# Kernel optimization log

Hardware: AMD Instinct MI355X
Metric: run time of the kernel (lower is better)

Reference implementation:

```python
import jax, jax.numpy as jnp
import numpy as np

H = 64

def _gru(x, Wih, Whh, bih, bhh):
    # x: [NB, L, D]; torch GRU gate order: r, z, n
    h0 = jnp.zeros((x.shape[0], Whh.shape[1]), x.dtype)
    def step(h, xt):
        gi = xt @ Wih.T + bih
        gh = h @ Whh.T + bhh
        ir, iz, inn = jnp.split(gi, 3, axis=-1)
        hr, hz, hn = jnp.split(gh, 3, axis=-1)
        r = jax.nn.sigmoid(ir + hr)
        z = jax.nn.sigmoid(iz + hz)
        n = jnp.tanh(inn + r * hn)
        h_new = (1.0 - z) * n + z * h
        return h_new, h_new
    hT, ys = jax.lax.scan(step, h0, jnp.swapaxes(x, 0, 1))
    return jnp.swapaxes(ys, 0, 1), hT  # outputs [NB,L,H], last hidden [NB,H]


def setup_inputs() -> dict:
    key = jax.random.key(0)
    ks = jax.random.split(key, 20)
    N, B, L, D = 2000, 8, 12, 2
    E = 16000
    s = 0.1
    return {
        "data": jax.random.normal(ks[0], (N, B, L, D), jnp.float32),
        "features": jax.random.normal(ks[1], (N, H), jnp.float32),
        "edge_index": jax.random.randint(ks[2], (2, E), 0, N, jnp.int64 if jax.config.jax_enable_x64 else jnp.int32),
        "Wih1": jax.random.normal(ks[3], (3 * H, D), jnp.float32) * s,
        "Whh1": jax.random.normal(ks[4], (3 * H, H), jnp.float32) * s,
        "bih1": jax.random.normal(ks[5], (3 * H,), jnp.float32) * s,
        "bhh1": jax.random.normal(ks[6], (3 * H,), jnp.float32) * s,
        "W1": jax.random.normal(ks[7], (16, 2 * H), jnp.float32) * s,
        "b1": jax.random.normal(ks[8], (16,), jnp.float32) * s,
        "W2": jax.random.normal(ks[9], (2, 16), jnp.float32) * s,
        "b2": jax.random.normal(ks[10], (2,), jnp.float32) * s,
        "W3": jax.random.normal(ks[11], (2 * H * H, 2), jnp.float32) * s,
        "b3": jax.random.normal(ks[12], (2 * H * H,), jnp.float32) * s,
        "Wih2": jax.random.normal(ks[13], (3 * H, H), jnp.float32) * s,
        "Whh2": jax.random.normal(ks[14], (3 * H, H), jnp.float32) * s,
        "bih2": jax.random.normal(ks[15], (3 * H,), jnp.float32) * s,
        "bhh2": jax.random.normal(ks[16], (3 * H,), jnp.float32) * s,
    }


def reference(data, features, edge_index, Wih1, Whh1, bih1, bhh1,
              W1, b1, W2, b2, W3, b3, Wih2, Whh2, bih2, bhh2):
    N, B, L, D = data.shape
    # --- first GRU over [N*B, L, D] ---
    out1, h1 = _gru(data.reshape(N * B, L, D), Wih1, Whh1, bih1, bhh1)
    out1 = out1.reshape(N, B, L, H)
    h1 = h1.reshape(N, B, H)
    # --- MetaGAT with self loops ---
    loops = jnp.arange(N, dtype=edge_index.dtype)
    src = jnp.concatenate([edge_index[0], loops])  # j (source)
    dst = jnp.concatenate([edge_index[1], loops])  # i (target)
    states_j = out1[src]                 # [E', B, L, H]
    states_i = out1[dst]
    feats = jnp.concatenate([features[dst], features[src]], axis=-1)  # [E', 2H]
    # per-edge MLP generating weights
    hdn = jax.nn.sigmoid(feats @ W1.T + b1)
    hdn = jax.nn.sigmoid(hdn @ W2.T + b2)
    w = (hdn @ W3.T + b3).reshape(-1, 2 * H, H)  # [E', 2H, H]
    states = jnp.concatenate([states_i, states_j], axis=-1)  # [E', B, L, 2H]
    alpha = jax.nn.leaky_relu(jnp.einsum('eblk,ekh->eblh', states, w))
    alpha = jax.nn.softmax(alpha, axis=1)  # softmax over batch dim, as in source
    msg = alpha * states_j                 # [E', B, L, H]
    agg = jax.ops.segment_sum(msg, dst, num_segments=N)
    out2 = jax.nn.relu(agg)                # [N, B, L, H]
    # --- second GRU ---
    _, h2 = _gru(out2.reshape(N * B, L, H), Wih2, Whh2, bih2, bhh2)
    h2 = h2.reshape(N, B, H)
    return h1, h2
```

## Files before the change

### kernel.cpp

```cpp
#include <hip/hip_runtime.h>
#include <hip/hip_bf16.h>

typedef unsigned short ushort_t;
typedef unsigned int uint_t;
typedef __attribute__((ext_vector_type(8))) short bf16x8;
typedef __attribute__((ext_vector_type(4))) float f32x4;

#define NNODE 2000
#define NB 8
#define LSEQ 12
#define HDIM 64
#define NEDGE 16000
#define NSEQ (NNODE * NB)
#define OUT1_ELEMS (NNODE * NB * LSEQ * HDIM)
#define OUT1_BYTES (OUT1_ELEMS * 2)
#define AGG_BYTES  (OUT1_ELEMS * 2)
#define SST 72
#define LOG2E 1.4426950408889634f

#define WFRAG_ELEMS (6 * 2 * 256 * 8)
#define G2FRAG_ELEMS (3 * 2 * 2 * 256 * 8)

__device__ __forceinline__ float bf1(ushort_t u) { return __uint_as_float(((uint_t)u) << 16); }
__device__ __forceinline__ ushort_t fbf(float f) {
    uint_t x = __float_as_uint(f);
    uint_t r = x + 0x7fffu + ((x >> 16) & 1u);
    return (ushort_t)(r >> 16);
}
__device__ __forceinline__ float sigm(float x) {
    return __builtin_amdgcn_rcpf(1.f + __expf(-x));
}
__device__ __forceinline__ float sigm2(float x) {
    return __builtin_amdgcn_rcpf(1.f + __builtin_amdgcn_exp2f(-x));
}
__device__ __forceinline__ float tanh2(float x) {
    return 2.f * __builtin_amdgcn_rcpf(1.f + __builtin_amdgcn_exp2f(-x)) - 1.f;
}


__global__ __launch_bounds__(256) void mega_kernel(
    const float* __restrict__ data, const float* __restrict__ Wih,
    const float* __restrict__ Whh, const float* __restrict__ bih,
    const float* __restrict__ bhh, ushort_t* __restrict__ out1,
    float* __restrict__ h1out,
    const int* __restrict__ edges, int* __restrict__ degree,
    int* __restrict__ rowstart, int* __restrict__ srcids,
    int* __restrict__ eids, int* __restrict__ order,
    const float* __restrict__ features,
    const float* __restrict__ W1, const float* __restrict__ b1,
    const float* __restrict__ W2, const float* __restrict__ b2,
    float* __restrict__ alphas,
    const float* __restrict__ W3, const float* __restrict__ b3,
    const float* __restrict__ Wih2, const float* __restrict__ Whh2,
    ushort_t* __restrict__ wfrag, ushort_t* __restrict__ g2frag)
{
    __shared__ ushort_t H[2][16][SST] __attribute__((aligned(16)));
    __shared__ float XD[16][26];
    __shared__ int hist[NNODE];
    __shared__ int wsum[4];
    __shared__ float m1[4][16];
    __shared__ int dh[64];

    const int bx = blockIdx.x;
    const int tid = threadIdx.x;

    if (bx == 5501) {
        {
            const int wv = tid >> 6, r = tid & 15, quad = (tid >> 4) & 3;
            const int n = wv * 16 + r;
#pragma unroll
            for (int ks = 0; ks < 2; ++ks) {
                ushort_t ta[8], tb[8], tc[8], ba[8], bb[8], bc[8];
#pragma unroll
                for (int jj = 0; jj < 8; ++jj) {
                    const int mt_ = (ks * 32 + quad * 8 + jj) * 64 + n;
                    float2 w2 = ((const float2*)W3)[mt_];
                    ta[jj] = fbf(w2.x * LOG2E); tb[jj] = fbf(w2.y * LOG2E);
                    tc[jj] = fbf(b3[mt_] * LOG2E);
                    const int mb_ = (64 + ks * 32 + quad * 8 + jj) * 64 + n;
                    float2 w2b = ((const float2*)W3)[mb_];
                    ba[jj] = fbf(w2b.x * LOG2E); bb[jj] = fbf(w2b.y * LOG2E);
                    bc[jj] = fbf(b3[mb_] * LOG2E);
                }
                *(uint4*)(wfrag + ((0 * 2 + ks) * 256 + tid) * 8) = *(uint4*)ta;
                *(uint4*)(wfrag + ((1 * 2 + ks) * 256 + tid) * 8) = *(uint4*)tb;
                *(uint4*)(wfrag + ((2 * 2 + ks) * 256 + tid) * 8) = *(uint4*)tc;
                *(uint4*)(wfrag + ((3 * 2 + ks) * 256 + tid) * 8) = *(uint4*)ba;
                *(uint4*)(wfrag + ((4 * 2 + ks) * 256 + tid) * 8) = *(uint4*)bb;
                *(uint4*)(wfrag + ((5 * 2 + ks) * 256 + tid) * 8) = *(uint4*)bc;
            }
        }
        {
            const int nw = tid >> 6, c = tid & 15, quad = (tid >> 4) & 3;
            const int j = nw * 16 + c;
#pragma unroll
            for (int g = 0; g < 3; ++g) {
                const float sc = (g == 2) ? 2.f * LOG2E : LOG2E;
                const int row = g * 64 + j;
#pragma unroll
                for (int ks = 0; ks < 2; ++ks) {
                    const float* wp = Whh2 + (row << 6) + ks * 32 + quad * 8;
                    float4 wa = *(const float4*)wp;
                    float4 wb = *(const float4*)(wp + 4);
                    ushort_t tmp[8];
                    tmp[0] = fbf(wa.x * sc); tmp[1] = fbf(wa.y * sc);
                    tmp[2] = fbf(wa.z * sc); tmp[3] = fbf(wa.w * sc);
                    tmp[4] = fbf(wb.x * sc); tmp[5] = fbf(wb.y * sc);
                    tmp[6] = fbf(wb.z * sc); tmp[7] = fbf(wb.w * sc);
                    *(uint4*)(g2frag + (((g * 2 + ks) * 2 + 0) * 256 + tid) * 8) = *(uint4*)tmp;
                    const float* wp2 = Wih2 + (row << 6) + ks * 32 + quad * 8;
                    float4 va = *(const float4*)wp2;
                    float4 vb = *(const float4*)(wp2 + 4);
                    tmp[0] = fbf(va.x * sc); tmp[1] = fbf(va.y * sc);
                    tmp[2] = fbf(va.z * sc); tmp[3] = fbf(va.w * sc);
                    tmp[4] = fbf(vb.x * sc); tmp[5] = fbf(vb.y * sc);
                    tmp[6] = fbf(vb.z * sc); tmp[7] = fbf(vb.w * sc);
                    *(uint4*)(g2frag + (((g * 2 + ks) * 2 + 1) * 256 + tid) * 8) = *(uint4*)tmp;
                }
            }
        }
        return;
    }

    if (bx == 1000) {
        for (int k = tid; k < NNODE; k += 256) hist[k] = 0;
        if (tid < 64) dh[tid] = 0;
        __syncthreads();
        for (int it = 0; it < 16; ++it) {
            const int e0 = it * 1024 + tid * 4;
            if (e0 + 3 < NEDGE) {
                int4 v4 = *(const int4*)(edges + NEDGE + e0);
                atomicAdd(&hist[v4.x], 1);
                atomicAdd(&hist[v4.y], 1);
                atomicAdd(&hist[v4.z], 1);
                atomicAdd(&hist[v4.w], 1);
            } else {
#pragma unroll
                for (int k = 0; k < 4; ++k) {
                    const int e = e0 + k;
                    if (e < NEDGE) atomicAdd(&hist[edges[NEDGE + e]], 1);
                }
            }
        }
        __syncthreads();
        const int lane = tid & 63, w = tid >> 6;
        int d[8];
        int s = 0;
#pragma unroll
        for (int q = 0; q < 8; ++q) {
            const int idx = tid * 8 + q;
            d[q] = (idx < NNODE) ? hist[idx] : 0;
            s += d[q];
        }
        int v = s;
#pragma unroll
        for (int off = 1; off < 64; off <<= 1) {
            int u = __shfl_up(v, off);
            if (lane >= off) v += u;
        }
        if (lane == 63) wsum[w] = v;
        __syncthreads();
        int base = 0;
        for (int k = 0; k < 4; ++k) if (k < w) base += wsum[k];
        int run = base + v - s;
        int rs8[8];
#pragma unroll
        for (int q = 0; q < 8; ++q) {
            const int idx = tid * 8 + q;
            if (idx < NNODE) {
                rs8[q] = run;
                rowstart[idx] = run;
                degree[idx] = d[q];
                run += d[q];
                atomicAdd(&dh[63 - min(d[q], 63)], 1);
            }
        }
        __syncthreads();
        if (tid == 0) {
            int acc = 0;
            for (int k = 0; k < 64; ++k) { const int c = dh[k]; dh[k] = acc; acc += c; }
        }
        __syncthreads();
#pragma unroll
        for (int q = 0; q < 8; ++q) {
            const int idx = tid * 8 + q;
            if (idx < NNODE) {
                const int pos = atomicAdd(&dh[63 - min(d[q], 63)], 1);
                order[pos] = idx;
            }
        }
        __syncthreads();
#pragma unroll
        for (int q = 0; q < 8; ++q) {
            const int idx = tid * 8 + q;
            if (idx < NNODE) hist[idx] = rs8[q];
        }
        __syncthreads();
        for (int it = 0; it < 16; ++it) {
            const int e0 = it * 1024 + tid * 4;
            if (e0 + 3 < NEDGE) {
                int4 dv4 = *(const int4*)(edges + NEDGE + e0);
                int4 sv4 = *(const int4*)(edges + e0);
                int pos;
                pos = atomicAdd(&hist[dv4.x], 1); srcids[pos] = sv4.x; eids[pos] = e0;
                pos = atomicAdd(&hist[dv4.y], 1); srcids[pos] = sv4.y; eids[pos] = e0 + 1;
                pos = atomicAdd(&hist[dv4.z], 1); srcids[pos] = sv4.z; eids[pos] = e0 + 2;
                pos = atomicAdd(&hist[dv4.w], 1); srcids[pos] = sv4.w; eids[pos] = e0 + 3;
            } else {
#pragma unroll
                for (int k = 0; k < 4; ++k) {
                    const int e = e0 + k;
                    if (e < NEDGE) {
                        const int pos = atomicAdd(&hist[edges[NEDGE + e]], 1);
                        srcids[pos] = edges[e];
                        eids[pos] = e;
                    }
                }
            }
        }
        return;
    }

    if (bx > 1000) {
        const int w = tid >> 6, lane = tid & 63;
        const int e = (bx - 1001) * 4 + w;
        int i, j;
        if (e < NEDGE) { j = edges[e]; i = edges[NEDGE + e]; }
        else { i = j = e - NEDGE; }
        const int o = lane >> 2, q = lane & 3;
        const float* fsrc = (q < 2) ? (features + i * 64 + q * 32)
                                    : (features + j * 64 + (q - 2) * 32);
        const float* wsrc = W1 + o * 128 + q * 32;
        const float4* f4 = (const float4*)fsrc;
        const float4* w4 = (const float4*)wsrc;
        float acc = 0.f;
#pragma unroll
        for (int k = 0; k < 8; ++k) {
            float4 a = f4[k], b = w4[k];
            acc = fmaf(a.x, b.x, acc);
            acc = fmaf(a.y, b.y, acc);
            acc = fmaf(a.z, b.z, acc);
            acc = fmaf(a.w, b.w, acc);
        }
        acc += __shfl_xor(acc, 1);
        acc += __shfl_xor(acc, 2);
        if (q == 0) m1[w][o] = sigm(acc + b1[o]);
        __syncthreads();
        if (lane < 32 && e < NEDGE + NNODE) {
            const int o2 = lane >> 4, k = lane & 15;
            float p = m1[w][k] * W2[o2 * 16 + k];
            p += __shfl_xor(p, 1);
            p += __shfl_xor(p, 2);
            p += __shfl_xor(p, 4);
            p += __shfl_xor(p, 8);
            if (k == 0) alphas[e * 2 + o2] = sigm(p + b2[o2]);
        }
        return;
    }

    const int nw = tid >> 6;
    const int c = tid & 15;
    const int quad = (tid >> 4) & 3;
    const int j = nw * 16 + c;
    const int s0 = bx * 16;
    const int crow = tid >> 4, ccol = (tid & 15) * 4;

    if (tid < 128) *(uint4*)&H[0][tid >> 3][(tid & 7) * 8] = uint4{0, 0, 0, 0};
#pragma unroll
    for (int p = 0; p < 2; ++p) {
        const int flat = p * 256 + tid;
        if (flat < 384) {
            const int sl = flat / 24, q = flat - sl * 24;
            XD[sl][q] = data[(s0 + sl) * 24 + q];
        }
    }

    bf16x8 Bh[3][2];
    float wi0[3], wi1[3], bi[3], bh[3];
#pragma unroll
    for (int g = 0; g < 3; ++g) {
        const float sc = (g == 2) ? 2.f * LOG2E : LOG2E;
        const int row = g * 64 + j;
        float2 wi = *(const float2*)(Wih + row * 2);
        wi0[g] = wi.x * sc; wi1[g] = wi.y * sc;
        bi[g] = bih[row] * sc; bh[g] = bhh[row] * sc;
#pragma unroll
        for (int ks = 0; ks < 2; ++ks) {
            const float* wp = Whh + (row << 6) + ks * 32 + quad * 8;
            float4 wa = *(const float4*)wp;
            float4 wb = *(const float4*)(wp + 4);
            ushort_t tmp[8];
            tmp[0] = fbf(wa.x * sc); tmp[1] = fbf(wa.y * sc);
            tmp[2] = fbf(wa.z * sc); tmp[3] = fbf(wa.w * sc);
            tmp[4] = fbf(wb.x * sc); tmp[5] = fbf(wb.y * sc);
            tmp[6] = fbf(wb.z * sc); tmp[7] = fbf(wb.w * sc);
            Bh[g][ks] = *(bf16x8*)tmp;
        }
    }

    float hold[4];
#pragma unroll
    for (int rg = 0; rg < 4; ++rg) hold[rg] = 0.f;

    for (int t = 0; t < LSEQ; ++t) {
        __syncthreads();
        const ushort_t (*Hr)[SST] = H[t & 1];
        ushort_t (*Hw)[SST] = H[1 - (t & 1)];
        bf16x8 a0 = *(const bf16x8*)&Hr[c][quad * 8];
        bf16x8 a1 = *(const bf16x8*)&Hr[c][32 + quad * 8];
        if (t > 0)
            *(uint2*)(out1 + (s0 + crow) * (LSEQ * HDIM) + (t - 1) * HDIM + ccol) =
                *(const uint2*)&Hr[crow][ccol];
        f32x4 gh[3];
#pragma unroll
        for (int g = 0; g < 3; ++g) {
            f32x4 acc = {0.f, 0.f, 0.f, 0.f};
            acc = __builtin_amdgcn_mfma_f32_16x16x32_bf16(a0, Bh[g][0], acc, 0, 0, 0);
            acc = __builtin_amdgcn_mfma_f32_16x16x32_bf16(a1, Bh[g][1], acc, 0, 0, 0);
            gh[g] = acc;
        }
#pragma unroll
        for (int rg = 0; rg < 4; ++rg) {
            const int sloc = quad * 4 + rg;
            float2 xp = *(const float2*)&XD[sloc][2 * t];
            float gr = bh[0] + gh[0][rg];
            float gz = bh[1] + gh[1][rg];
            float gn = bh[2] + gh[2][rg];
            float ir = bi[0] + wi0[0] * xp.x + wi1[0] * xp.y;
            float iz = bi[1] + wi0[1] * xp.x + wi1[1] * xp.y;
            float in = bi[2] + wi0[2] * xp.x + wi1[2] * xp.y;
            float r = sigm2(ir + gr);
            float z = sigm2(iz + gz);
            float n = tanh2(in + r * gn);
            float hv = (1.f - z) * n + z * hold[rg];
            hold[rg] = hv;
            Hw[sloc][j] = fbf(hv);
        }
    }
    __syncthreads();
    *(uint2*)(out1 + (s0 + crow) * (LSEQ * HDIM) + (LSEQ - 1) * HDIM + ccol) =
        *(const uint2*)&H[LSEQ & 1][crow][ccol];
#pragma unroll
    for (int rg = 0; rg < 4; ++rg) {
        const int sloc = quad * 4 + rg;
        h1out[(s0 + sloc) * HDIM + j] = hold[rg];
    }
}

__global__ __launch_bounds__(256) void gat_csr_kernel(
    const ushort_t* __restrict__ out1,
    const int* __restrict__ degree, const int* __restrict__ rowstart,
    const int* __restrict__ srcids, const int* __restrict__ eids,
    const int* __restrict__ order,
    const float* __restrict__ alphas,
    const ushort_t* __restrict__ wfrag,
    ushort_t* __restrict__ agg)
{
    __shared__ ushort_t POOL[4][32][SST] __attribute__((aligned(16)));

    const int tid = threadIdx.x;
    const int i = order[blockIdx.x];
    const int mh = blockIdx.y;
    const int deg = degree[i];
    const int rs = rowstart[i];

    const int wv = tid >> 6;
    const int r = tid & 15;
    const int quad = (tid >> 4) & 3;
    const int n = wv * 16 + r;

    const float2 aSelf = *(const float2*)(alphas + (NEDGE + i) * 2);

    int glo[2], lso[2];
#pragma unroll
    for (int p = 0; p < 2; ++p) {
        const int u = p * 256 + tid;
        const int rr = u >> 4, c4 = u & 15;
        const int b = rr & 7, l = (rr >> 3) + 4 * mh;
        glo[p] = (b * 12 + l) * 64 + c4 * 4;
        lso[p] = rr * SST + c4 * 4;
    }
    int afo[2][2];
#pragma unroll
    for (int mt = 0; mt < 2; ++mt) {
        afo[mt][0] = (mt * 16 + r) * SST + quad * 8;
        afo[mt][1] = afo[mt][0] + 32;
    }
    int cbo[2];
#pragma unroll
    for (int mt = 0; mt < 2; ++mt)
        cbo[mt] = (mt * 16 + quad * 4) * SST + (n & ~1);
    const uint_t shamt = (n & 1) ? 0u : 16u;

    const ushort_t* pi = out1 + i * (NB * LSEQ * HDIM);
    ushort_t* const sbase = &POOL[0][0][0];
    ushort_t* const Si = sbase;

#pragma unroll
    for (int p = 0; p < 2; ++p)
        *(uint2*)(Si + lso[p]) = *(const uint2*)(pi + glo[p]);

    bf16x8 WtA[2], WtB[2], WtC[2], WbA[2], WbB[2], WbC[2];
#pragma unroll
    for (int ks = 0; ks < 2; ++ks) {
        WtA[ks] = *(const bf16x8*)(wfrag + ((0 * 2 + ks) * 256 + tid) * 8);
        WtB[ks] = *(const bf16x8*)(wfrag + ((1 * 2 + ks) * 256 + tid) * 8);
        WtC[ks] = *(const bf16x8*)(wfrag + ((2 * 2 + ks) * 256 + tid) * 8);
        WbA[ks] = *(const bf16x8*)(wfrag + ((3 * 2 + ks) * 256 + tid) * 8);
        WbB[ks] = *(const bf16x8*)(wfrag + ((4 * 2 + ks) * 256 + tid) * 8);
        WbC[ks] = *(const bf16x8*)(wfrag + ((5 * 2 + ks) * 256 + tid) * 8);
    }

    __syncthreads();

    f32x4 PA[2], PB[2], PC[2];
#pragma unroll
    for (int mt = 0; mt < 2; ++mt) {
        bf16x8 af0 = *(const bf16x8*)(Si + afo[mt][0]);
        bf16x8 af1 = *(const bf16x8*)(Si + afo[mt][1]);
        f32x4 pa = {0.f, 0.f, 0.f, 0.f};
        f32x4 pb = {0.f, 0.f, 0.f, 0.f};
        f32x4 pc = {0.f, 0.f, 0.f, 0.f};
        pa = __builtin_amdgcn_mfma_f32_16x16x32_bf16(af0, WtA[0], pa, 0, 0, 0);
        pa = __builtin_amdgcn_mfma_f32_16x16x32_bf16(af1, WtA[1], pa, 0, 0, 0);
        pb = __builtin_amdgcn_mfma_f32_16x16x32_bf16(af0, WtB[0], pb, 0, 0, 0);
        pb = __builtin_amdgcn_mfma_f32_16x16x32_bf16(af1, WtB[1], pb, 0, 0, 0);
        pc = __builtin_amdgcn_mfma_f32_16x16x32_bf16(af0, WtC[0], pc, 0, 0, 0);
        pc = __builtin_amdgcn_mfma_f32_16x16x32_bf16(af1, WtC[1], pc, 0, 0, 0);
        PA[mt] = pa; PB[mt] = pb; PC[mt] = pc;
    }

    float accN[2][4];
#pragma unroll
    for (int mt = 0; mt < 2; ++mt)
#pragma unroll
        for (int g2 = 0; g2 < 4; ++g2) accN[mt][g2] = 0.f;

    auto process = [&](const ushort_t* SB, float2 a01) {
#pragma unroll
        for (int mt = 0; mt < 2; ++mt) {
            bf16x8 aj0 = *(const bf16x8*)(SB + afo[mt][0]);
            bf16x8 aj1 = *(const bf16x8*)(SB + afo[mt][1]);
            const uint_t* dp = (const uint_t*)(SB + cbo[mt]);
            uint_t d0 = dp[0], d1 = dp[36], d2 = dp[72], d3 = dp[108];
            f32x4 aA = PA[mt], aB = PB[mt], aC = PC[mt];
            aA = __builtin_amdgcn_mfma_f32_16x16x32_bf16(aj0, WbA[0], aA, 0, 0, 0);
            aA = __builtin_amdgcn_mfma_f32_16x16x32_bf16(aj1, WbA[1], aA, 0, 0, 0);
            aB = __builtin_amdgcn_mfma_f32_16x16x32_bf16(aj0, WbB[0], aB, 0, 0, 0);
            aB = __builtin_amdgcn_mfma_f32_16x16x32_bf16(aj1, WbB[1], aB, 0, 0, 0);
            aC = __builtin_amdgcn_mfma_f32_16x16x32_bf16(aj0, WbC[0], aC, 0, 0, 0);
            aC = __builtin_amdgcn_mfma_f32_16x16x32_bf16(aj1, WbC[1], aC, 0, 0, 0);
            float v[4];
            float s = 0.f;
#pragma unroll
            for (int g2 = 0; g2 < 4; ++g2) {
                float x = fmaf(a01.x, aA[g2], fmaf(a01.y, aB[g2], aC[g2]));
                x = fmaxf(x, 0.01f * x);
                v[g2] = __builtin_amdgcn_exp2f(x);
                s += v[g2];
            }
            s += __shfl_xor(s, 16);
            const float inv = __builtin_amdgcn_rcpf(s);
            uint_t dd[4] = {d0, d1, d2, d3};
#pragma unroll
            for (int g2 = 0; g2 < 4; ++g2) {
                const float sj = __uint_as_float((dd[g2] << shamt) & 0xFFFF0000u);
                accN[mt][g2] += v[g2] * inv * sj;
            }
        }
    };

    int eA1 = 0, eB1 = 0, eA2 = 0, eB2 = 0, sa2 = 0, sb2 = 0;
    float2 aA_cur = float2{0.f, 0.f}, aB_cur = float2{0.f, 0.f};
    if (deg >= 1) aA_cur = *(const float2*)(alphas + eids[rs] * 2);
    if (deg >= 2) aB_cur = *(const float2*)(alphas + eids[rs + 1] * 2);
    if (deg >= 3) eA1 = eids[rs + 2];
    if (deg >= 4) eB1 = eids[rs + 3];
    if (deg >= 5) { eA2 = eids[rs + 4]; sa2 = srcids[rs + 4]; }
    if (deg >= 6) { eB2 = eids[rs + 5]; sb2 = srcids[rs + 5]; }

    uint2 pfEA[2], pfEB[2], pfOA[2], pfOB[2];
    {
        const ushort_t* pA = out1 + ((deg >= 1) ? srcids[rs]     : 0) * (NB * LSEQ * HDIM);
        const ushort_t* pB = out1 + ((deg >= 2) ? srcids[rs + 1] : 0) * (NB * LSEQ * HDIM);
        const ushort_t* pC = out1 + ((deg >= 3) ? srcids[rs + 2] : 0) * (NB * LSEQ * HDIM);
        const ushort_t* pD = out1 + ((deg >= 4) ? srcids[rs + 3] : 0) * (NB * LSEQ * HDIM);
#pragma unroll
        for (int p = 0; p < 2; ++p) {
            pfEA[p] = *(const uint2*)(pA + glo[p]);
            pfEB[p] = *(const uint2*)(pB + glo[p]);
            pfOA[p] = *(const uint2*)(pC + glo[p]);
            pfOB[p] = *(const uint2*)(pD + glo[p]);
        }
    }

    process(Si, aSelf);
    __syncthreads();

    const int npairs = (deg + 1) >> 1;
    for (int pk = 0; pk < npairs; ++pk) {
        const int base = pk * 2;
        ushort_t* SA = sbase + (2 * (pk & 1)) * (32 * SST);
        ushort_t* SB = SA + 32 * SST;

        if ((pk & 1) == 0) {
#pragma unroll
            for (int p = 0; p < 2; ++p) {
                *(uint2*)(SA + lso[p]) = pfEA[p];
                *(uint2*)(SB + lso[p]) = pfEB[p];
            }
            if (base + 4 < deg) {
                const ushort_t* pA = out1 + sa2 * (NB * LSEQ * HDIM);
#pragma unroll
                for (int p = 0; p < 2; ++p) pfEA[p] = *(const uint2*)(pA + glo[p]);
            }
            if (base + 5 < deg) {
                const ushort_t* pB = out1 + sb2 * (NB * LSEQ * HDIM);
#pragma unroll
                for (int p = 0; p < 2; ++p) pfEB[p] = *(const uint2*)(pB + glo[p]);
            }
        } else {
#pragma unroll
            for (int p = 0; p < 2; ++p) {
                *(uint2*)(SA + lso[p]) = pfOA[p];
                *(uint2*)(SB + lso[p]) = pfOB[p];
            }
            if (base + 4 < deg) {
                const ushort_t* pA = out1 + sa2 * (NB * LSEQ * HDIM);
#pragma unroll
                for (int p = 0; p < 2; ++p) pfOA[p] = *(const uint2*)(pA + glo[p]);
            }
            if (base + 5 < deg) {
                const ushort_t* pB = out1 + sb2 * (NB * LSEQ * HDIM);
#pragma unroll
                for (int p = 0; p < 2; ++p) pfOB[p] = *(const uint2*)(pB + glo[p]);
            }
        }

        int sa_nw = 0, sb_nw = 0, e3A = 0, e3B = 0;
        if (base + 6 < deg) { sa_nw = srcids[rs + base + 6]; e3A = eids[rs + base + 6]; }
        if (base + 7 < deg) { sb_nw = srcids[rs + base + 7]; e3B = eids[rs + base + 7]; }
        float2 aA_n = float2{0.f, 0.f}, aB_n = float2{0.f, 0.f};
        if (base + 2 < deg) aA_n = *(const float2*)(alphas + eA1 * 2);
        if (base + 3 < deg) aB_n = *(const float2*)(alphas + eB1 * 2);

        __syncthreads();

        process(SA, aA_cur);
        if (base + 1 < deg) process(SB, aB_cur);

        aA_cur = aA_n; aB_cur = aB_n;
        eA1 = eA2; eB1 = eB2; eA2 = e3A; eB2 = e3B;
        sa2 = sa_nw; sb2 = sb_nw;
    }

#pragma unroll
    for (int mt = 0; mt < 2; ++mt)
#pragma unroll
        for (int g2 = 0; g2 < 4; ++g2) {
            const int gr = mh * 32 + mt * 16 + quad * 4 + g2;
            const int b = gr & 7, l = gr >> 3;
            agg[(i * 96 + b * 12 + l) * 64 + n] = fbf(accN[mt][g2]);
        }
}

__global__ __launch_bounds__(256) void gru2_kernel(
    const ushort_t* __restrict__ agg, const ushort_t* __restrict__ g2frag,
    const float* __restrict__ bih, const float* __restrict__ bhh,
    float* __restrict__ h2out)
{
    __shared__ ushort_t H[2][16][SST] __attribute__((aligned(16)));
    __shared__ ushort_t X[2][16][SST] __attribute__((aligned(16)));

    const int tid = threadIdx.x;
    const int nw = tid >> 6;
    const int c = tid & 15;
    const int quad = (tid >> 4) & 3;
    const int j = nw * 16 + c;
    const int s0 = blockIdx.x * 16;
    const int sl = tid >> 3, k0 = (tid & 7) * 8;

    if (tid < 128) *(uint4*)&H[0][tid >> 3][(tid & 7) * 8] = uint4{0, 0, 0, 0};

    bf16x8 Bh[3][2], Bi[3][2];
    float bi[3], bh[3];
#pragma unroll
    for (int g = 0; g < 3; ++g) {
        const float sc = (g == 2) ? 2.f * LOG2E : LOG2E;
        const int row = g * 64 + j;
        bi[g] = bih[row] * sc; bh[g] = bhh[row] * sc;
#pragma unroll
        for (int ks = 0; ks < 2; ++ks) {
            Bh[g][ks] = *(const bf16x8*)(g2frag + (((g * 2 + ks) * 2 + 0) * 256 + tid) * 8);
            Bi[g][ks] = *(const bf16x8*)(g2frag + (((g * 2 + ks) * 2 + 1) * 256 + tid) * 8);
        }
    }

    float hold[4];
#pragma unroll
    for (int rg = 0; rg < 4; ++rg) hold[rg] = 0.f;

    if (tid < 128) {
        ushort_t xr[8];
        *(uint4*)xr = *(const uint4*)(agg + (s0 + sl) * (LSEQ * HDIM) + k0);
        ushort_t xs[8];
#pragma unroll
        for (int q = 0; q < 8; ++q) xs[q] = (xr[q] & 0x8000u) ? (ushort_t)0 : xr[q];
        *(uint4*)&X[0][sl][k0] = *(uint4*)xs;
    }

    for (int t = 0; t < LSEQ; ++t) {
        __syncthreads();
        const int rb = t & 1, wb = 1 - rb;
        bf16x8 ah0 = *(const bf16x8*)&H[rb][c][quad * 8];
        bf16x8 ah1 = *(const bf16x8*)&H[rb][c][32 + quad * 8];
        bf16x8 ax0 = *(const bf16x8*)&X[rb][c][quad * 8];
        bf16x8 ax1 = *(const bf16x8*)&X[rb][c][32 + quad * 8];

        ushort_t xr[8];
        if (t < LSEQ - 1 && tid < 128)
            *(uint4*)xr = *(const uint4*)(agg + (s0 + sl) * (LSEQ * HDIM) +
                                          (t + 1) * HDIM + k0);

        f32x4 gh[3], gi[3];
#pragma unroll
        for (int g = 0; g < 3; ++g) {
            f32x4 acc = {0.f, 0.f, 0.f, 0.f};
            acc = __builtin_amdgcn_mfma_f32_16x16x32_bf16(ah0, Bh[g][0], acc, 0, 0, 0);
            acc = __builtin_amdgcn_mfma_f32_16x16x32_bf16(ah1, Bh[g][1], acc, 0, 0, 0);
            gh[g] = acc;
            f32x4 acc2 = {0.f, 0.f, 0.f, 0.f};
            acc2 = __builtin_amdgcn_mfma_f32_16x16x32_bf16(ax0, Bi[g][0], acc2, 0, 0, 0);
            acc2 = __builtin_amdgcn_mfma_f32_16x16x32_bf16(ax1, Bi[g][1], acc2, 0, 0, 0);
            gi[g] = acc2;
        }
#pragma unroll
        for (int rg = 0; rg < 4; ++rg) {
            const int sloc = quad * 4 + rg;
            float r = sigm2(bi[0] + gi[0][rg] + bh[0] + gh[0][rg]);
            float z = sigm2(bi[1] + gi[1][rg] + bh[1] + gh[1][rg]);
            float n = tanh2(bi[2] + gi[2][rg] + r * (bh[2] + gh[2][rg]));
            float hv = (1.f - z) * n + z * hold[rg];
            hold[rg] = hv;
            H[wb][sloc][j] = fbf(hv);
        }
        if (t < LSEQ - 1 && tid < 128) {
            ushort_t xs[8];
#pragma unroll
            for (int q = 0; q < 8; ++q) xs[q] = (xr[q] & 0x8000u) ? (ushort_t)0 : xr[q];
            *(uint4*)&X[wb][sl][k0] = *(uint4*)xs;
        }
    }
#pragma unroll
    for (int rg = 0; rg < 4; ++rg) {
        const int sloc = quad * 4 + rg;
        h2out[(s0 + sloc) * HDIM + j] = hold[rg];
    }
}

extern "C" void kernel_launch(void* const* d_in, const int* in_sizes, int n_in,
                              void* d_out, int out_size, void* d_ws, size_t ws_size,
                              hipStream_t stream)
{
    const float* data     = (const float*)d_in[0];
    const float* features = (const float*)d_in[1];
    const int*   edges    = (const int*)d_in[2];
    const float* Wih1     = (const float*)d_in[3];
    const float* Whh1     = (const float*)d_in[4];
    const float* bih1     = (const float*)d_in[5];
    const float* bhh1     = (const float*)d_in[6];
    const float* W1       = (const float*)d_in[7];
    const float* b1       = (const float*)d_in[8];
    const float* W2       = (const float*)d_in[9];
    const float* b2       = (const float*)d_in[10];
    const float* W3       = (const float*)d_in[11];
    const float* b3       = (const float*)d_in[12];
    const float* Wih2     = (const float*)d_in[13];
    const float* Whh2     = (const float*)d_in[14];
    const float* bih2     = (const float*)d_in[15];
    const float* bhh2     = (const float*)d_in[16];

    float*    out  = (float*)d_out;
    char*     ws   = (char*)d_ws;
    ushort_t* out1 = (ushort_t*)ws;
    ushort_t* agg  = (ushort_t*)(ws + OUT1_BYTES);
    int*      meta = (int*)(ws + OUT1_BYTES + AGG_BYTES);
    int*   degree   = meta;
    int*   rowstart = meta + NNODE;
    int*   srcids   = meta + 2 * NNODE;
    int*   eids     = meta + 2 * NNODE + NEDGE;
    int*   order    = meta + 2 * NNODE + 2 * NEDGE;
    float* alphas   = (float*)(meta + 3 * NNODE + 2 * NEDGE);
    ushort_t* wfrag  = (ushort_t*)((char*)alphas + 36000 * 4);
    ushort_t* g2frag = wfrag + WFRAG_ELEMS;

    mega_kernel<<<1001 + 4500 + 1, 256, 0, stream>>>(
        data, Wih1, Whh1, bih1, bhh1, out1, out,
        edges, degree, rowstart, srcids, eids, order,
        features, W1, b1, W2, b2, alphas,
        W3, b3, Wih2, Whh2, wfrag, g2frag);
    gat_csr_kernel<<<dim3(NNODE, 3), 256, 0, stream>>>(out1, degree, rowstart, srcids,
                                                       eids, order, alphas, wfrag, agg);
    gru2_kernel<<<NSEQ / 16, 256, 0, stream>>>(agg, g2frag, bih2, bhh2,
                                               out + NNODE * NB * HDIM);
}
```

Measured before the change: 230.7 us.

## Process GAT neighbor edges in groups of four with double-buffered LDS

Restructures the per-node GAT edge loop to stage four neighbor tiles per iteration instead of two. LDS is doubled to 8 buffers and prefetches of the next four source tiles are issued after the barrier. This halves the number of __syncthreads per node and exposes more memory-level parallelism for the gathers. The cost is more registers for the prefetched tiles, more LDS per block (lower occupancy), and some wasted work on low-degree nodes.

```diff
diff --git a/kernel.cpp b/kernel.cpp
--- a/kernel.cpp
+++ b/kernel.cpp
@@ -356,7 +356,7 @@
     const ushort_t* __restrict__ wfrag,
     ushort_t* __restrict__ agg)
 {
-    __shared__ ushort_t POOL[4][32][SST] __attribute__((aligned(16)));
+    __shared__ ushort_t POOL[8][32][SST] __attribute__((aligned(16)));
 
     const int tid = threadIdx.x;
     const int i = order[blockIdx.x];
@@ -409,6 +409,25 @@
         WbA[ks] = *(const bf16x8*)(wfrag + ((3 * 2 + ks) * 256 + tid) * 8);
         WbB[ks] = *(const bf16x8*)(wfrag + ((4 * 2 + ks) * 256 + tid) * 8);
         WbC[ks] = *(const bf16x8*)(wfrag + ((5 * 2 + ks) * 256 + tid) * 8);
+    }
+
+    float2 aC[4];
+    int e1[4], s1[4];
+#pragma unroll
+    for (int k = 0; k < 4; ++k) {
+        aC[k] = float2{0.f, 0.f};
+        if (k < deg) aC[k] = *(const float2*)(alphas + eids[rs + k] * 2);
+        const int idx = 4 + k;
+        e1[k] = 0; s1[k] = 0;
+        if (idx < deg) { e1[k] = eids[rs + idx]; s1[k] = srcids[rs + idx]; }
+    }
+
+    uint2 pf[4][2];
+#pragma unroll
+    for (int k = 0; k < 4; ++k) {
+        const ushort_t* pA = out1 + ((k < deg) ? srcids[rs + k] : 0) * (NB * LSEQ * HDIM);
+#pragma unroll
+        for (int p = 0; p < 2; ++p) pf[k][p] = *(const uint2*)(pA + glo[p]);
     }
 
     __syncthreads();
@@ -443,18 +462,18 @@
             bf16x8 aj1 = *(const bf16x8*)(SB + afo[mt][1]);
             const uint_t* dp = (const uint_t*)(SB + cbo[mt]);
             uint_t d0 = dp[0], d1 = dp[36], d2 = dp[72], d3 = dp[108];
-            f32x4 aA = PA[mt], aB = PB[mt], aC = PC[mt];
+            f32x4 aA = PA[mt], aB = PB[mt], aC_ = PC[mt];
             aA = __builtin_amdgcn_mfma_f32_16x16x32_bf16(aj0, WbA[0], aA, 0, 0, 0);
             aA = __builtin_amdgcn_mfma_f32_16x16x32_bf16(aj1, WbA[1], aA, 0, 0, 0);
             aB = __builtin_amdgcn_mfma_f32_16x16x32_bf16(aj0, WbB[0], aB, 0, 0, 0);
             aB = __builtin_amdgcn_mfma_f32_16x16x32_bf16(aj1, WbB[1], aB, 0, 0, 0);
-            aC = __builtin_amdgcn_mfma_f32_16x16x32_bf16(aj0, WbC[0], aC, 0, 0, 0);
-            aC = __builtin_amdgcn_mfma_f32_16x16x32_bf16(aj1, WbC[1], aC, 0, 0, 0);
+            aC_ = __builtin_amdgcn_mfma_f32_16x16x32_bf16(aj0, WbC[0], aC_, 0, 0, 0);
+            aC_ = __builtin_amdgcn_mfma_f32_16x16x32_bf16(aj1, WbC[1], aC_, 0, 0, 0);
             float v[4];
             float s = 0.f;
 #pragma unroll
             for (int g2 = 0; g2 < 4; ++g2) {
-                float x = fmaf(a01.x, aA[g2], fmaf(a01.y, aB[g2], aC[g2]));
+                float x = fmaf(a01.x, aA[g2], fmaf(a01.y, aB[g2], aC_[g2]));
                 x = fmaxf(x, 0.01f * x);
                 v[g2] = __builtin_amdgcn_exp2f(x);
                 s += v[g2];
@@ -470,88 +489,52 @@
         }
     };
 
-    int eA1 = 0, eB1 = 0, eA2 = 0, eB2 = 0, sa2 = 0, sb2 = 0;
-    float2 aA_cur = float2{0.f, 0.f}, aB_cur = float2{0.f, 0.f};
-    if (deg >= 1) aA_cur = *(const float2*)(alphas + eids[rs] * 2);
-    if (deg >= 2) aB_cur = *(const float2*)(alphas + eids[rs + 1] * 2);
-    if (deg >= 3) eA1 = eids[rs + 2];
-    if (deg >= 4) eB1 = eids[rs + 3];
-    if (deg >= 5) { eA2 = eids[rs + 4]; sa2 = srcids[rs + 4]; }
-    if (deg >= 6) { eB2 = eids[rs + 5]; sb2 = srcids[rs + 5]; }
-
-    uint2 pfEA[2], pfEB[2], pfOA[2], pfOB[2];
-    {
-        const ushort_t* pA = out1 + ((deg >= 1) ? srcids[rs]     : 0) * (NB * LSEQ * HDIM);
-        const ushort_t* pB = out1 + ((deg >= 2) ? srcids[rs + 1] : 0) * (NB * LSEQ * HDIM);
-        const ushort_t* pC = out1 + ((deg >= 3) ? srcids[rs + 2] : 0) * (NB * LSEQ * HDIM);
-        const ushort_t* pD = out1 + ((deg >= 4) ? srcids[rs + 3] : 0) * (NB * LSEQ * HDIM);
-#pragma unroll
-        for (int p = 0; p < 2; ++p) {
-            pfEA[p] = *(const uint2*)(pA + glo[p]);
-            pfEB[p] = *(const uint2*)(pB + glo[p]);
-            pfOA[p] = *(const uint2*)(pC + glo[p]);
-            pfOB[p] = *(const uint2*)(pD + glo[p]);
-        }
-    }
-
     process(Si, aSelf);
     __syncthreads();
 
-    const int npairs = (deg + 1) >> 1;
-    for (int pk = 0; pk < npairs; ++pk) {
-        const int base = pk * 2;
-        ushort_t* SA = sbase + (2 * (pk & 1)) * (32 * SST);
-        ushort_t* SB = SA + 32 * SST;
-
-        if ((pk & 1) == 0) {
-#pragma unroll
-            for (int p = 0; p < 2; ++p) {
-                *(uint2*)(SA + lso[p]) = pfEA[p];
-                *(uint2*)(SB + lso[p]) = pfEB[p];
-            }
-            if (base + 4 < deg) {
-                const ushort_t* pA = out1 + sa2 * (NB * LSEQ * HDIM);
-#pragma unroll
-                for (int p = 0; p < 2; ++p) pfEA[p] = *(const uint2*)(pA + glo[p]);
-            }
-            if (base + 5 < deg) {
-                const ushort_t* pB = out1 + sb2 * (NB * LSEQ * HDIM);
-#pragma unroll
-                for (int p = 0; p < 2; ++p) pfEB[p] = *(const uint2*)(pB + glo[p]);
-            }
-        } else {
-#pragma unroll
-            for (int p = 0; p < 2; ++p) {
-                *(uint2*)(SA + lso[p]) = pfOA[p];
-                *(uint2*)(SB + lso[p]) = pfOB[p];
-            }
-            if (base + 4 < deg) {
-                const ushort_t* pA = out1 + sa2 * (NB * LSEQ * HDIM);
-#pragma unroll
-                for (int p = 0; p < 2; ++p) pfOA[p] = *(const uint2*)(pA + glo[p]);
-            }
-            if (base + 5 < deg) {
-                const ushort_t* pB = out1 + sb2 * (NB * LSEQ * HDIM);
-#pragma unroll
-                for (int p = 0; p < 2; ++p) pfOB[p] = *(const uint2*)(pB + glo[p]);
-            }
-        }
-
-        int sa_nw = 0, sb_nw = 0, e3A = 0, e3B = 0;
-        if (base + 6 < deg) { sa_nw = srcids[rs + base + 6]; e3A = eids[rs + base + 6]; }
-        if (base + 7 < deg) { sb_nw = srcids[rs + base + 7]; e3B = eids[rs + base + 7]; }
-        float2 aA_n = float2{0.f, 0.f}, aB_n = float2{0.f, 0.f};
-        if (base + 2 < deg) aA_n = *(const float2*)(alphas + eA1 * 2);
-        if (base + 3 < deg) aB_n = *(const float2*)(alphas + eB1 * 2);
-
-        __syncthreads();
-
-        process(SA, aA_cur);
-        if (base + 1 < deg) process(SB, aB_cur);
-
-        aA_cur = aA_n; aB_cur = aB_n;
-        eA1 = eA2; eB1 = eB2; eA2 = e3A; eB2 = e3B;
-        sa2 = sa_nw; sb2 = sb_nw;
+    const int nquads = (deg + 3) >> 2;
+    for (int qk = 0; qk < nquads; ++qk) {
+        const int base = qk * 4;
+        ushort_t* S0 = sbase + ((qk & 1) * 4) * (32 * SST);
+
+#pragma unroll
+        for (int k = 0; k < 4; ++k) {
+            if (base + k < deg) {
+                ushort_t* Sk = S0 + k * (32 * SST);
+#pragma unroll
+                for (int p = 0; p < 2; ++p) *(uint2*)(Sk + lso[p]) = pf[k][p];
+            }
+        }
+
+        float2 aN[4];
+        int e2[4], s2[4];
+#pragma unroll
+        for (int k = 0; k < 4; ++k) {
+            aN[k] = float2{0.f, 0.f};
+            if (base + 4 + k < deg) aN[k] = *(const float2*)(alphas + e1[k] * 2);
+            const int idx = base + 8 + k;
+            e2[k] = 0; s2[k] = 0;
+            if (idx < deg) { e2[k] = eids[rs + idx]; s2[k] = srcids[rs + idx]; }
+        }
+
+        __syncthreads();
+
+#pragma unroll
+        for (int k = 0; k < 4; ++k) {
+            if (base + 4 + k < deg) {
+                const ushort_t* pA = out1 + s1[k] * (NB * LSEQ * HDIM);
+#pragma unroll
+                for (int p = 0; p < 2; ++p) pf[k][p] = *(const uint2*)(pA + glo[p]);
+            }
+        }
+
+#pragma unroll
+        for (int k = 0; k < 4; ++k) {
+            if (base + k < deg) process(S0 + k * (32 * SST), aC[k]);
+        }
+
+#pragma unroll
+        for (int k = 0; k < 4; ++k) { aC[k] = aN[k]; e1[k] = e2[k]; s1[k] = s2[k]; }
     }
 
 #pragma unroll
```

New measurement: 230.7 us. Within noise of the previous version (-0.0%).
